# Performance work log

Measured on AMD Instinct MI355X. Metric: run time of the kernel, lower is better.

Reference implementation:

```python
import jax, jax.numpy as jnp
import numpy as np

B, S, HID = 2, 4096, 640
NH, NKV, HD = 4, 1, 256
SCALING = 256.0 ** -0.5
SOFTCAP = 50.0
WINDOW = 512
EPS = 1e-6
ROPE_THETA = 10000.0  # local (sliding) rope base in Gemma3


def _rope_tables(seq_len, dim, theta):
    inv_freq = 1.0 / (theta ** (np.arange(0, dim, 2, dtype=np.float32) / dim))  # [dim/2]
    t = np.arange(seq_len, dtype=np.float32)
    freqs = np.outer(t, inv_freq)                      # [S, dim/2]
    emb = np.concatenate([freqs, freqs], axis=-1)      # [S, dim]
    return np.cos(emb)[None], np.sin(emb)[None]        # [1, S, dim]


def _sliding_causal_mask(b, s, window):
    i = np.arange(s)[:, None]
    j = np.arange(s)[None, :]
    allowed = (j <= i) & (j > i - window)              # causal + sliding window
    mask = np.where(allowed, 0.0, -1e9).astype(np.float32)
    return np.broadcast_to(mask[None, None], (b, 1, s, s)).copy()


def setup_inputs() -> dict:
    key = jax.random.key(0)
    ks = jax.random.split(key, 8)
    cos_np, sin_np = _rope_tables(S, HD, ROPE_THETA)
    return {
        "hidden_states": jax.random.normal(ks[0], (B, S, HID), jnp.float32),
        "cos": jnp.asarray(cos_np),
        "sin": jnp.asarray(sin_np),
        "attention_mask": jnp.asarray(_sliding_causal_mask(B, S, WINDOW)),
        "Wq": jax.random.normal(ks[1], (HID, NH * HD), jnp.float32) * 0.02,
        "Wk": jax.random.normal(ks[2], (HID, NKV * HD), jnp.float32) * 0.02,
        "Wv": jax.random.normal(ks[3], (HID, NKV * HD), jnp.float32) * 0.02,
        "Wo": jax.random.normal(ks[4], (NH * HD, HID), jnp.float32) * 0.02,
        "q_norm_w": jax.random.normal(ks[5], (HD,), jnp.float32) * 0.02,
        "k_norm_w": jax.random.normal(ks[6], (HD,), jnp.float32) * 0.02,
    }


def _rms_norm(x, w):
    var = jnp.mean(jnp.square(x), axis=-1, keepdims=True)
    return x * jax.lax.rsqrt(var + EPS) * (1.0 + w)


def _rotate_half(x):
    x1, x2 = jnp.split(x, 2, axis=-1)
    return jnp.concatenate([-x2, x1], axis=-1)


def _apply_rope(x, cos, sin):
    # x: [B, H, S, D]; cos/sin: [1, S, D] -> unsqueeze head dim
    c = cos[:, None, :, :]
    s = sin[:, None, :, :]
    return x * c + _rotate_half(x) * s


def reference(hidden_states, cos, sin, attention_mask, Wq, Wk, Wv, Wo, q_norm_w, k_norm_w):
    b, s, _ = hidden_states.shape
    # projections (no bias)
    q = (hidden_states @ Wq).reshape(b, s, NH, HD).transpose(0, 2, 1, 3)   # [B,NH,S,D]
    k = (hidden_states @ Wk).reshape(b, s, NKV, HD).transpose(0, 2, 1, 3)  # [B,1,S,D]
    v = (hidden_states @ Wv).reshape(b, s, NKV, HD).transpose(0, 2, 1, 3)  # [B,1,S,D]
    # per-head RMSNorm on q/k
    q = _rms_norm(q, q_norm_w)
    k = _rms_norm(k, k_norm_w)
    # RoPE
    q = _apply_rope(q, cos, sin)
    k = _apply_rope(k, cos, sin)
    # GQA: single kv head broadcast to all query heads
    k2 = k[:, 0]  # [B,S,D]
    v2 = v[:, 0]  # [B,S,D]
    scores = jnp.einsum('bhqd,bkd->bhqk', q, k2) * SCALING
    scores = SOFTCAP * jnp.tanh(scores / SOFTCAP)          # logit softcapping
    scores = scores + attention_mask                        # causal + sliding window
    attn = jax.nn.softmax(scores, axis=-1)
    out = jnp.einsum('bhqk,bkd->bhqd', attn, v2)            # [B,NH,S,D]
    out = out.transpose(0, 2, 1, 3).reshape(b, s, NH * HD)  # [B,S,NH*D]
    return out @ Wo                                         # [B,S,HID]
```

## Files before the change

kernel.cpp:

```cpp
#include <hip/hip_runtime.h>

typedef unsigned short u16;
typedef unsigned int u32;

typedef __attribute__((ext_vector_type(8)))  short bf16x8;
typedef __attribute__((ext_vector_type(4)))  float f32x4;

__device__ __forceinline__ float b2f(u16 u) {
    union { unsigned int i; float f; } v; v.i = ((unsigned int)u) << 16; return v.f;
}
__device__ __forceinline__ u16 f2b(float f) {
    union { float ff; unsigned int i; } v; v.ff = f;
    unsigned int x = v.i;
    return (u16)((x + 0x7fffu + ((x >> 16) & 1u)) >> 16);
}
__device__ __forceinline__ bool detect_bf16(const void* cosT) {
    return ((*(const u32*)cosT) & 0xffffu) == 0x3f80u;
}
__device__ __forceinline__ float4 ld4(const void* p, size_t off, bool isbf) {
    if (isbf) {
        ushort4 v = *(const ushort4*)((const u16*)p + off);
        return make_float4(b2f(v.x), b2f(v.y), b2f(v.z), b2f(v.w));
    }
    return *(const float4*)((const float*)p + off);
}
__device__ __forceinline__ float lds1(const void* p, size_t off, bool isbf) {
    return isbf ? b2f(((const u16*)p)[off]) : ((const float*)p)[off];
}
__device__ __forceinline__ void gll16(const void* g, void* l) {
    __builtin_amdgcn_global_load_lds(
        (const __attribute__((address_space(1))) u32*)g,
        (__attribute__((address_space(3))) u32*)l, 16, 0, 0);
}
__device__ __forceinline__ float capmask(float sdot, int i, int j) {
    float v = sdot * (0.0625f / 50.0f);
    v = fminf(fmaxf(v, -10.0f), 10.0f);
    float e = __expf(2.0f * v);
    float c = 50.0f * (e - 1.0f) / (e + 1.0f);
    bool allowed = (j <= i) && (j > i - 512);
    return allowed ? c : -1e30f;
}

__global__ __launch_bounds__(256) void prep(
    const void* __restrict__ hidden,
    const void* __restrict__ Wq, const void* __restrict__ Wk,
    const void* __restrict__ Wv, const void* __restrict__ Wo,
    const void* __restrict__ cosT,
    u16* __restrict__ Hb, u16* __restrict__ WT, u16* __restrict__ WoT)
{
    const bool isbf = detect_bf16(cosT);
    __shared__ float T[32][33];
    int id = blockIdx.x;
    if (id < 2560) {
        size_t base = ((size_t)id * 256 + threadIdx.x) * 8;
        if (isbf) {
            *(uint4*)(Hb + base) = *(const uint4*)((const u16*)hidden + base);
        } else {
            float4 a = ld4(hidden, base, false);
            float4 b = ld4(hidden, base + 4, false);
            uint4 o;
            o.x = (u32)f2b(a.x) | ((u32)f2b(a.y) << 16);
            o.y = (u32)f2b(a.z) | ((u32)f2b(a.w) << 16);
            o.z = (u32)f2b(b.x) | ((u32)f2b(b.y) << 16);
            o.w = (u32)f2b(b.z) | ((u32)f2b(b.w) << 16);
            *(uint4*)(Hb + base) = o;
        }
        return;
    }
    id -= 2560;
    const int tx = threadIdx.x & 31, ty = threadIdx.x >> 5;
    if (id < 960) {
        const int n0 = (id % 48) * 32, k0 = (id / 48) * 32;
        const void* src; int ldw, nof;
        if (n0 < 1024)      { src = Wq; ldw = 1024; nof = n0; }
        else if (n0 < 1280) { src = Wk; ldw = 256;  nof = n0 - 1024; }
        else                { src = Wv; ldw = 256;  nof = n0 - 1280; }
#pragma unroll
        for (int j = 0; j < 4; j++)
            T[ty + 8 * j][tx] = lds1(src, (size_t)(k0 + ty + 8 * j) * ldw + nof + tx, isbf);
        __syncthreads();
#pragma unroll
        for (int j = 0; j < 4; j++)
            WT[(size_t)(n0 + ty + 8 * j) * 640 + k0 + tx] = f2b(T[tx][ty + 8 * j]);
    } else {
        id -= 960;
        const int k0 = (id & 31) * 32, n0 = (id >> 5) * 32;
#pragma unroll
        for (int j = 0; j < 4; j++)
            T[ty + 8 * j][tx] = lds1(Wo, (size_t)(k0 + ty + 8 * j) * 640 + n0 + tx, isbf);
        __syncthreads();
#pragma unroll
        for (int j = 0; j < 4; j++)
            WoT[(size_t)(n0 + ty + 8 * j) * 1024 + k0 + tx] = f2b(T[tx][ty + 8 * j]);
    }
}

__global__ __launch_bounds__(256) void qkv_gemm(
    const u16* __restrict__ Hb, const u16* __restrict__ WT,
    u16* __restrict__ Qb, u16* __restrict__ Kb, u16* __restrict__ Vtg)
{
    const int n0 = blockIdx.x * 128, m0 = blockIdx.y * 128;
    const int t = threadIdx.x, w = t >> 6, lane = t & 63;
    const int l15 = lane & 15, quad = lane >> 4;
    const int wm = (w & 1) * 64, wn = (w >> 1) * 64;

    __shared__ __align__(16) u16 Ah[128][32];
    __shared__ __align__(16) u16 Bh[128][32];
    __shared__ __align__(16) u16 Sc[128][132];

    f32x4 acc[4][4];
#pragma unroll
    for (int i = 0; i < 4; i++)
#pragma unroll
        for (int j = 0; j < 4; j++) acc[i][j] = (f32x4)0.0f;

    for (int kb = 0; kb < 640; kb += 32) {
        __syncthreads();
#pragma unroll
        for (int i = 0; i < 2; i++) {
            int ci = t + 256 * i, m = ci >> 2, c = ci & 3;
            gll16(Hb + (size_t)(m0 + m) * 640 + kb + c * 8, (char*)&Ah[0][0] + ci * 16);
            gll16(WT + (size_t)(n0 + m) * 640 + kb + c * 8, (char*)&Bh[0][0] + ci * 16);
        }
        __syncthreads();
        bf16x8 af[4], bfr[4];
#pragma unroll
        for (int mi = 0; mi < 4; mi++)
            af[mi] = *(const bf16x8*)&Ah[wm + mi * 16 + l15][quad * 8];
#pragma unroll
        for (int ni = 0; ni < 4; ni++)
            bfr[ni] = *(const bf16x8*)&Bh[wn + ni * 16 + l15][quad * 8];
#pragma unroll
        for (int mi = 0; mi < 4; mi++)
#pragma unroll
            for (int ni = 0; ni < 4; ni++)
                acc[mi][ni] = __builtin_amdgcn_mfma_f32_16x16x32_bf16(
                    af[mi], bfr[ni], acc[mi][ni], 0, 0, 0);
    }

    if (n0 >= 1280) {
        const int bb = m0 >> 12, sblk = m0 & 4095;
#pragma unroll
        for (int mi = 0; mi < 4; mi++)
#pragma unroll
            for (int ni = 0; ni < 4; ni++) {
                int vd = n0 + wn + ni * 16 + l15 - 1280;
                int sb = sblk + wm + mi * 16 + quad * 4;
                ushort4 vv = make_ushort4(f2b(acc[mi][ni][0]), f2b(acc[mi][ni][1]),
                                          f2b(acc[mi][ni][2]), f2b(acc[mi][ni][3]));
                *(ushort4*)(Vtg + (size_t)bb * 1048576 + (size_t)vd * 4096 + sb) = vv;
            }
        return;
    }

    __syncthreads();
#pragma unroll
    for (int mi = 0; mi < 4; mi++)
#pragma unroll
        for (int ni = 0; ni < 4; ni++)
#pragma unroll
            for (int r = 0; r < 4; r++)
                Sc[wm + mi * 16 + quad * 4 + r][wn + ni * 16 + l15] = f2b(acc[mi][ni][r]);
    __syncthreads();

    u16* dst; int ldo, coff;
    if (n0 < 1024) { dst = Qb; ldo = 1024; coff = n0; }
    else           { dst = Kb; ldo = 256;  coff = n0 - 1024; }
#pragma unroll
    for (int i = 0; i < 8; i++) {
        int idx = t + 256 * i, r = idx >> 4, c = idx & 15;
        *(uint4*)(dst + (size_t)(m0 + r) * ldo + coff + c * 8) = *(const uint4*)&Sc[r][c * 8];
    }
}

__global__ __launch_bounds__(320) void norm_rope(
    u16* __restrict__ Qb, u16* __restrict__ Kb,
    const void* __restrict__ cosT, const void* __restrict__ sinT,
    const void* __restrict__ qw, const void* __restrict__ kw)
{
    const bool isbf = detect_bf16(cosT);
    const int row = blockIdx.x, s = row & 4095;
    const int g = threadIdx.x >> 6, lane = threadIdx.x & 63, d0 = lane * 4;

    u16* p; const void* w;
    if (g < 4) { p = Qb + (size_t)row * 1024 + g * 256 + d0; w = qw; }
    else       { p = Kb + (size_t)row * 256 + d0;            w = kw; }

    ushort4 xv = *(const ushort4*)p;
    float x0 = b2f(xv.x), x1 = b2f(xv.y), x2 = b2f(xv.z), x3 = b2f(xv.w);
    float ssum = x0 * x0 + x1 * x1 + x2 * x2 + x3 * x3;
#pragma unroll
    for (int off = 32; off > 0; off >>= 1) ssum += __shfl_xor(ssum, off, 64);
    float rs = rsqrtf(ssum * (1.0f / 256.0f) + 1e-6f);

    float4 wv = ld4(w, d0, isbf);
    float n0 = x0 * rs * (1.0f + wv.x);
    float n1 = x1 * rs * (1.0f + wv.y);
    float n2 = x2 * rs * (1.0f + wv.z);
    float n3 = x3 * rs * (1.0f + wv.w);

    float o0 = __shfl_xor(n0, 32, 64);
    float o1 = __shfl_xor(n1, 32, 64);
    float o2 = __shfl_xor(n2, 32, 64);
    float o3 = __shfl_xor(n3, 32, 64);
    float sgn = (lane < 32) ? -1.0f : 1.0f;

    float4 cv = ld4(cosT, (size_t)s * 256 + d0, isbf);
    float4 sv = ld4(sinT, (size_t)s * 256 + d0, isbf);
    *(ushort4*)p = make_ushort4(
        f2b(n0 * cv.x + sgn * o0 * sv.x), f2b(n1 * cv.y + sgn * o1 * sv.y),
        f2b(n2 * cv.z + sgn * o2 * sv.z), f2b(n3 * cv.w + sgn * o3 * sv.w));
}

__global__ __launch_bounds__(256, 2) void attn_mfma(
    const u16* __restrict__ Qb, const u16* __restrict__ Kb,
    const u16* __restrict__ Vtg, u16* __restrict__ AO)
{
    const int bx = blockIdx.x;
    const int q0 = (((bx & 7) << 5) + (bx >> 3)) * 16;
    const int b  = blockIdx.y;
    const int t = threadIdx.x, h = t >> 6, lane = t & 63;
    const int l15 = lane & 15, quad = lane >> 4;

    __shared__ __align__(16) u16 Ks[32][264];
    __shared__ __align__(16) u16 Vt[256][40];
    __shared__ __align__(16) u16 Pr[4][16][40];
    __shared__ float l_s[4][16];

    bf16x8 qf[8];
    {
        const u16* qp = Qb + ((size_t)(b * 4096 + q0 + l15)) * 1024 + h * 256 + quad * 8;
#pragma unroll
        for (int s = 0; s < 8; s++) qf[s] = *(const bf16x8*)(qp + s * 32);
    }

    f32x4 o[16];
#pragma unroll
    for (int i = 0; i < 16; i++) o[i] = (f32x4)0.0f;
    float lp[4] = {0.f, 0.f, 0.f, 0.f};

    const int lo = q0 - 511;
    const int jb0 = lo > 0 ? (lo >> 5) << 5 : 0;
    const int jb1 = (q0 + 15) & ~31;

    const u16* kbase = Kb + (size_t)b * 4096 * 256;
    const u16* vbase = Vtg + (size_t)b * 1048576;

    for (int jb = jb0; jb <= jb1; jb += 32) {
        __syncthreads();
#pragma unroll
        for (int i = 0; i < 4; i++) {
            int ci = t + 256 * i;
            *(uint4*)&Ks[ci >> 5][(ci & 31) * 8] =
                *(const uint4*)(kbase + (size_t)(jb + (ci >> 5)) * 256 + (ci & 31) * 8);
            *(uint4*)&Vt[ci >> 2][(ci & 3) * 8] =
                *(const uint4*)(vbase + (size_t)(ci >> 2) * 4096 + jb + (ci & 3) * 8);
        }
        __syncthreads();

        f32x4 s0 = (f32x4)0.0f, s1 = (f32x4)0.0f;
#pragma unroll
        for (int ds = 0; ds < 8; ds++) {
            bf16x8 kf0 = *(const bf16x8*)&Ks[l15][ds * 32 + quad * 8];
            bf16x8 kf1 = *(const bf16x8*)&Ks[16 + l15][ds * 32 + quad * 8];
            s0 = __builtin_amdgcn_mfma_f32_16x16x32_bf16(qf[ds], kf0, s0, 0, 0, 0);
            s1 = __builtin_amdgcn_mfma_f32_16x16x32_bf16(qf[ds], kf1, s1, 0, 0, 0);
        }
        const int j0 = jb + l15;
#pragma unroll
        for (int r = 0; r < 4; r++) {
            int qi = q0 + quad * 4 + r;
            float p0 = __expf(capmask(s0[r], qi, j0));
            float p1 = __expf(capmask(s1[r], qi, j0 + 16));
            u16 pb0 = f2b(p0), pb1 = f2b(p1);
            Pr[h][quad * 4 + r][l15]      = pb0;
            Pr[h][quad * 4 + r][16 + l15] = pb1;
            lp[r] += b2f(pb0) + b2f(pb1);
        }
        __threadfence_block();
        bf16x8 pf = *(const bf16x8*)&Pr[h][l15][quad * 8];
#pragma unroll
        for (int mt = 0; mt < 16; mt++) {
            bf16x8 vf = *(const bf16x8*)&Vt[mt * 16 + l15][quad * 8];
            o[mt] = __builtin_amdgcn_mfma_f32_16x16x32_bf16(vf, pf, o[mt], 0, 0, 0);
        }
    }

#pragma unroll
    for (int r = 0; r < 4; r++) {
        float v = lp[r];
        v += __shfl_xor(v, 1, 64); v += __shfl_xor(v, 2, 64);
        v += __shfl_xor(v, 4, 64); v += __shfl_xor(v, 8, 64);
        lp[r] = v;
    }
    if (l15 == 0) {
#pragma unroll
        for (int r = 0; r < 4; r++) l_s[h][quad * 4 + r] = lp[r];
    }
    __threadfence_block();
    __syncthreads();
    const float inv = 1.0f / l_s[h][l15];

    u16* aop = AO + ((size_t)(b * 4096 + q0 + l15)) * 1024 + h * 256 + quad * 4;
#pragma unroll
    for (int mt = 0; mt < 16; mt++) {
        *(ushort4*)(aop + mt * 16) = make_ushort4(
            f2b(o[mt][0] * inv), f2b(o[mt][1] * inv),
            f2b(o[mt][2] * inv), f2b(o[mt][3] * inv));
    }
}

__global__ __launch_bounds__(256) void out_gemm(
    const u16* __restrict__ AO, const u16* __restrict__ WoT,
    const void* __restrict__ cosT, void* __restrict__ outp)
{
    const bool isbf = detect_bf16(cosT);
    const int n0 = blockIdx.x * 64, m0 = blockIdx.y * 128;
    const int t = threadIdx.x, w = t >> 6, lane = t & 63;
    const int l15 = lane & 15, quad = lane >> 4;
    const int wm = (w & 1) * 64, wn = (w >> 1) * 32;

    __shared__ __align__(16) u16 Ah[128][32];
    __shared__ __align__(16) u16 Bh[64][32];
    __shared__ __align__(16) float Scf[128][68];

    f32x4 acc[4][2];
#pragma unroll
    for (int i = 0; i < 4; i++)
#pragma unroll
        for (int j = 0; j < 2; j++) acc[i][j] = (f32x4)0.0f;

    for (int kb = 0; kb < 1024; kb += 32) {
        __syncthreads();
#pragma unroll
        for (int i = 0; i < 2; i++) {
            int ci = t + 256 * i, m = ci >> 2, c = ci & 3;
            gll16(AO + (size_t)(m0 + m) * 1024 + kb + c * 8, (char*)&Ah[0][0] + ci * 16);
        }
        {
            int m = t >> 2, c = t & 3;
            gll16(WoT + (size_t)(n0 + m) * 1024 + kb + c * 8, (char*)&Bh[0][0] + t * 16);
        }
        __syncthreads();
        bf16x8 af[4], bfr[2];
#pragma unroll
        for (int mi = 0; mi < 4; mi++)
            af[mi] = *(const bf16x8*)&Ah[wm + mi * 16 + l15][quad * 8];
#pragma unroll
        for (int ni = 0; ni < 2; ni++)
            bfr[ni] = *(const bf16x8*)&Bh[wn + ni * 16 + l15][quad * 8];
#pragma unroll
        for (int mi = 0; mi < 4; mi++)
#pragma unroll
            for (int ni = 0; ni < 2; ni++)
                acc[mi][ni] = __builtin_amdgcn_mfma_f32_16x16x32_bf16(
                    af[mi], bfr[ni], acc[mi][ni], 0, 0, 0);
    }

    __syncthreads();
#pragma unroll
    for (int mi = 0; mi < 4; mi++)
#pragma unroll
        for (int ni = 0; ni < 2; ni++)
#pragma unroll
            for (int r = 0; r < 4; r++)
                Scf[wm + mi * 16 + quad * 4 + r][wn + ni * 16 + l15] = acc[mi][ni][r];
    __syncthreads();

    if (isbf) {
#pragma unroll
        for (int i = 0; i < 4; i++) {
            int idx = t + 256 * i, r = idx >> 3, c = idx & 7;
            ushort4 lo4 = make_ushort4(
                f2b(Scf[r][c * 8 + 0]), f2b(Scf[r][c * 8 + 1]),
                f2b(Scf[r][c * 8 + 2]), f2b(Scf[r][c * 8 + 3]));
            ushort4 hi4 = make_ushort4(
                f2b(Scf[r][c * 8 + 4]), f2b(Scf[r][c * 8 + 5]),
                f2b(Scf[r][c * 8 + 6]), f2b(Scf[r][c * 8 + 7]));
            u16* p = (u16*)outp + (size_t)(m0 + r) * 640 + n0 + c * 8;
            *(ushort4*)p = lo4; *(ushort4*)(p + 4) = hi4;
        }
    } else {
#pragma unroll
        for (int i = 0; i < 8; i++) {
            int idx = t + 256 * i, r = idx >> 4, c = idx & 15;
            float4 v = *(const float4*)&Scf[r][c * 4];
            *(float4*)((float*)outp + (size_t)(m0 + r) * 640 + n0 + c * 4) = v;
        }
    }
}

extern "C" void kernel_launch(void* const* d_in, const int* in_sizes, int n_in,
                              void* d_out, int out_size, void* d_ws, size_t ws_size,
                              hipStream_t stream) {
    const void* hidden = d_in[0];
    const void* cosT   = d_in[1];
    const void* sinT   = d_in[2];
    const void* Wq     = d_in[4];
    const void* Wk     = d_in[5];
    const void* Wv     = d_in[6];
    const void* Wo     = d_in[7];
    const void* qw     = d_in[8];
    const void* kw     = d_in[9];

    char* ws = (char*)d_ws;
    u16* Hb  = (u16*)ws;
    u16* WT  = (u16*)(ws + 10485760);
    u16* AO  = (u16*)ws;
    u16* WoT = (u16*)(ws + 16777216);
    u16* Qb  = (u16*)(ws + 18087936);
    u16* Kb  = (u16*)(ws + 34865152);
    u16* Vtg = (u16*)(ws + 39059456);

    prep<<<dim3(4160), 256, 0, stream>>>(hidden, Wq, Wk, Wv, Wo, cosT, Hb, WT, WoT);
    qkv_gemm<<<dim3(12, 64), 256, 0, stream>>>(Hb, WT, Qb, Kb, Vtg);
    norm_rope<<<dim3(8192), 320, 0, stream>>>(Qb, Kb, cosT, sinT, qw, kw);
    attn_mfma<<<dim3(256, 2), 256, 0, stream>>>(Qb, Kb, Vtg, AO);
    out_gemm<<<dim3(10, 64), 256, 0, stream>>>(AO, WoT, cosT, d_out);
}
```

Baseline: 330.7 us.

## Double-buffer GEMM LDS loads and widen attention blocks to 32 query rows

New measurement: 322.3 us. -2.5%, faster.

```diff
diff --git a/kernel.cpp b/kernel.cpp
--- a/kernel.cpp
+++ b/kernel.cpp
@@ -104,9 +104,7 @@
     const int l15 = lane & 15, quad = lane >> 4;
     const int wm = (w & 1) * 64, wn = (w >> 1) * 64;
 
-    __shared__ __align__(16) u16 Ah[128][32];
-    __shared__ __align__(16) u16 Bh[128][32];
-    __shared__ __align__(16) u16 Sc[128][132];
+    __shared__ __align__(16) char smem[33792];
 
     f32x4 acc[4][4];
 #pragma unroll
@@ -114,15 +112,28 @@
 #pragma unroll
         for (int j = 0; j < 4; j++) acc[i][j] = (f32x4)0.0f;
 
-    for (int kb = 0; kb < 640; kb += 32) {
-        __syncthreads();
-#pragma unroll
-        for (int i = 0; i < 2; i++) {
-            int ci = t + 256 * i, m = ci >> 2, c = ci & 3;
-            gll16(Hb + (size_t)(m0 + m) * 640 + kb + c * 8, (char*)&Ah[0][0] + ci * 16);
-            gll16(WT + (size_t)(n0 + m) * 640 + kb + c * 8, (char*)&Bh[0][0] + ci * 16);
-        }
-        __syncthreads();
+#pragma unroll
+    for (int i = 0; i < 2; i++) {
+        int ci = t + 256 * i, m = ci >> 2, c = ci & 3;
+        gll16(Hb + (size_t)(m0 + m) * 640 + c * 8, smem + ci * 16);
+        gll16(WT + (size_t)(n0 + m) * 640 + c * 8, smem + 8192 + ci * 16);
+    }
+    __syncthreads();
+
+    for (int it = 0; it < 20; ++it) {
+        const int kb = it * 32;
+        char* cur = smem + (it & 1) * 16384;
+        if (it < 19) {
+            char* nxt = smem + ((it + 1) & 1) * 16384;
+#pragma unroll
+            for (int i = 0; i < 2; i++) {
+                int ci = t + 256 * i, m = ci >> 2, c = ci & 3;
+                gll16(Hb + (size_t)(m0 + m) * 640 + kb + 32 + c * 8, nxt + ci * 16);
+                gll16(WT + (size_t)(n0 + m) * 640 + kb + 32 + c * 8, nxt + 8192 + ci * 16);
+            }
+        }
+        const u16 (*Ah)[32] = (const u16 (*)[32])cur;
+        const u16 (*Bh)[32] = (const u16 (*)[32])(cur + 8192);
         bf16x8 af[4], bfr[4];
 #pragma unroll
         for (int mi = 0; mi < 4; mi++)
@@ -136,6 +147,7 @@
             for (int ni = 0; ni < 4; ni++)
                 acc[mi][ni] = __builtin_amdgcn_mfma_f32_16x16x32_bf16(
                     af[mi], bfr[ni], acc[mi][ni], 0, 0, 0);
+        __syncthreads();
     }
 
     if (n0 >= 1280) {
@@ -153,7 +165,7 @@
         return;
     }
 
-    __syncthreads();
+    u16 (*Sc)[132] = (u16 (*)[132])smem;
 #pragma unroll
     for (int mi = 0; mi < 4; mi++)
 #pragma unroll
@@ -212,24 +224,26 @@
         f2b(n2 * cv.z + sgn * o2 * sv.z), f2b(n3 * cv.w + sgn * o3 * sv.w));
 }
 
-__global__ __launch_bounds__(256, 2) void attn_mfma(
+__global__ __launch_bounds__(512, 2) void attn_mfma(
     const u16* __restrict__ Qb, const u16* __restrict__ Kb,
     const u16* __restrict__ Vtg, u16* __restrict__ AO)
 {
     const int bx = blockIdx.x;
-    const int q0 = (((bx & 7) << 5) + (bx >> 3)) * 16;
+    const int q0 = (((bx & 7) << 4) + (bx >> 3)) * 32;
     const int b  = blockIdx.y;
-    const int t = threadIdx.x, h = t >> 6, lane = t & 63;
+    const int t = threadIdx.x, w = t >> 6, lane = t & 63;
+    const int h = w & 3, qh = w >> 2;
     const int l15 = lane & 15, quad = lane >> 4;
+    const int qbase = q0 + qh * 16;
 
     __shared__ __align__(16) u16 Ks[32][264];
     __shared__ __align__(16) u16 Vt[256][40];
-    __shared__ __align__(16) u16 Pr[4][16][40];
-    __shared__ float l_s[4][16];
+    __shared__ __align__(16) u16 Pr[8][16][40];
+    __shared__ float l_s[8][16];
 
     bf16x8 qf[8];
     {
-        const u16* qp = Qb + ((size_t)(b * 4096 + q0 + l15)) * 1024 + h * 256 + quad * 8;
+        const u16* qp = Qb + ((size_t)(b * 4096 + qbase + l15)) * 1024 + h * 256 + quad * 8;
 #pragma unroll
         for (int s = 0; s < 8; s++) qf[s] = *(const bf16x8*)(qp + s * 32);
     }
@@ -241,7 +255,7 @@
 
     const int lo = q0 - 511;
     const int jb0 = lo > 0 ? (lo >> 5) << 5 : 0;
-    const int jb1 = (q0 + 15) & ~31;
+    const int jb1 = (q0 + 31) & ~31;
 
     const u16* kbase = Kb + (size_t)b * 4096 * 256;
     const u16* vbase = Vtg + (size_t)b * 1048576;
@@ -249,8 +263,8 @@
     for (int jb = jb0; jb <= jb1; jb += 32) {
         __syncthreads();
 #pragma unroll
-        for (int i = 0; i < 4; i++) {
-            int ci = t + 256 * i;
+        for (int i = 0; i < 2; i++) {
+            int ci = t + 512 * i;
             *(uint4*)&Ks[ci >> 5][(ci & 31) * 8] =
                 *(const uint4*)(kbase + (size_t)(jb + (ci >> 5)) * 256 + (ci & 31) * 8);
             *(uint4*)&Vt[ci >> 2][(ci & 3) * 8] =
@@ -269,16 +283,16 @@
         const int j0 = jb + l15;
 #pragma unroll
         for (int r = 0; r < 4; r++) {
-            int qi = q0 + quad * 4 + r;
+            int qi = qbase + quad * 4 + r;
             float p0 = __expf(capmask(s0[r], qi, j0));
             float p1 = __expf(capmask(s1[r], qi, j0 + 16));
             u16 pb0 = f2b(p0), pb1 = f2b(p1);
-            Pr[h][quad * 4 + r][l15]      = pb0;
-            Pr[h][quad * 4 + r][16 + l15] = pb1;
+            Pr[w][quad * 4 + r][l15]      = pb0;
+            Pr[w][quad * 4 + r][16 + l15] = pb1;
             lp[r] += b2f(pb0) + b2f(pb1);
         }
         __threadfence_block();
-        bf16x8 pf = *(const bf16x8*)&Pr[h][l15][quad * 8];
+        bf16x8 pf = *(const bf16x8*)&Pr[w][l15][quad * 8];
 #pragma unroll
         for (int mt = 0; mt < 16; mt++) {
             bf16x8 vf = *(const bf16x8*)&Vt[mt * 16 + l15][quad * 8];
@@ -295,13 +309,13 @@
     }
     if (l15 == 0) {
 #pragma unroll
-        for (int r = 0; r < 4; r++) l_s[h][quad * 4 + r] = lp[r];
+        for (int r = 0; r < 4; r++) l_s[w][quad * 4 + r] = lp[r];
     }
     __threadfence_block();
     __syncthreads();
-    const float inv = 1.0f / l_s[h][l15];
-
-    u16* aop = AO + ((size_t)(b * 4096 + q0 + l15)) * 1024 + h * 256 + quad * 4;
+    const float inv = 1.0f / l_s[w][l15];
+
+    u16* aop = AO + ((size_t)(b * 4096 + qbase + l15)) * 1024 + h * 256 + quad * 4;
 #pragma unroll
     for (int mt = 0; mt < 16; mt++) {
         *(ushort4*)(aop + mt * 16) = make_ushort4(
@@ -320,9 +334,7 @@
     const int l15 = lane & 15, quad = lane >> 4;
     const int wm = (w & 1) * 64, wn = (w >> 1) * 32;
 
-    __shared__ __align__(16) u16 Ah[128][32];
-    __shared__ __align__(16) u16 Bh[64][32];
-    __shared__ __align__(16) float Scf[128][68];
+    __shared__ __align__(16) char smem[34816];
 
     f32x4 acc[4][2];
 #pragma unroll
@@ -330,18 +342,32 @@
 #pragma unroll
         for (int j = 0; j < 2; j++) acc[i][j] = (f32x4)0.0f;
 
-    for (int kb = 0; kb < 1024; kb += 32) {
-        __syncthreads();
+    {
 #pragma unroll
         for (int i = 0; i < 2; i++) {
             int ci = t + 256 * i, m = ci >> 2, c = ci & 3;
-            gll16(AO + (size_t)(m0 + m) * 1024 + kb + c * 8, (char*)&Ah[0][0] + ci * 16);
-        }
-        {
+            gll16(AO + (size_t)(m0 + m) * 1024 + c * 8, smem + ci * 16);
+        }
+        int m = t >> 2, c = t & 3;
+        gll16(WoT + (size_t)(n0 + m) * 1024 + c * 8, smem + 8192 + t * 16);
+    }
+    __syncthreads();
+
+    for (int it = 0; it < 32; ++it) {
+        const int kb = it * 32;
+        char* cur = smem + (it & 1) * 12288;
+        if (it < 31) {
+            char* nxt = smem + ((it + 1) & 1) * 12288;
+#pragma unroll
+            for (int i = 0; i < 2; i++) {
+                int ci = t + 256 * i, m = ci >> 2, c = ci & 3;
+                gll16(AO + (size_t)(m0 + m) * 1024 + kb + 32 + c * 8, nxt + ci * 16);
+            }
             int m = t >> 2, c = t & 3;
-            gll16(WoT + (size_t)(n0 + m) * 1024 + kb + c * 8, (char*)&Bh[0][0] + t * 16);
-        }
-        __syncthreads();
+            gll16(WoT + (size_t)(n0 + m) * 1024 + kb + 32 + c * 8, nxt + 8192 + t * 16);
+        }
+        const u16 (*Ah)[32] = (const u16 (*)[32])cur;
+        const u16 (*Bh)[32] = (const u16 (*)[32])(cur + 8192);
         bf16x8 af[4], bfr[2];
 #pragma unroll
         for (int mi = 0; mi < 4; mi++)
@@ -355,9 +381,10 @@
             for (int ni = 0; ni < 2; ni++)
                 acc[mi][ni] = __builtin_amdgcn_mfma_f32_16x16x32_bf16(
                     af[mi], bfr[ni], acc[mi][ni], 0, 0, 0);
-    }
-
-    __syncthreads();
+        __syncthreads();
+    }
+
+    float (*Scf)[68] = (float (*)[68])smem;
 #pragma unroll
     for (int mi = 0; mi < 4; mi++)
 #pragma unroll
@@ -415,6 +442,6 @@
     prep<<<dim3(4160), 256, 0, stream>>>(hidden, Wq, Wk, Wv, Wo, cosT, Hb, WT, WoT);
     qkv_gemm<<<dim3(12, 64), 256, 0, stream>>>(Hb, WT, Qb, Kb, Vtg);
     norm_rope<<<dim3(8192), 320, 0, stream>>>(Qb, Kb, cosT, sinT, qw, kw);
-    attn_mfma<<<dim3(256, 2), 256, 0, stream>>>(Qb, Kb, Vtg, AO);
+    attn_mfma<<<dim3(128, 2), 512, 0, stream>>>(Qb, Kb, Vtg, AO);
     out_gemm<<<dim3(10, 64), 256, 0, stream>>>(AO, WoT, cosT, d_out);
 }
```
